# Kernel optimization log

Hardware: AMD Instinct MI355X
Metric: run time of the kernel (lower is better)

The kernel has to match this reference:

```python
import jax, jax.numpy as jnp
import numpy as np

EPS = 1e-6
CHUNK = 128  # chunk size for the chunked causal recurrence


def elu_feature_map(x):
    # fast_transformers default feature map: elu(x) + 1
    return jax.nn.elu(x) + 1.0


def causal_dot_product(Q, K, V):
    """out[l] = Q[l] @ sum_{l' <= l} K[l']^T V[l'].
    Q, K: (N, L, H, E); V: (N, L, H, D) -> (N, L, H, D).
    Chunked parallel recurrence: intra-chunk masked attention + inter-chunk state.
    """
    N, L, H, E = Q.shape
    D = V.shape[-1]
    C = CHUNK
    nc = L // C

    def to_chunks(x):
        # (N, L, H, F) -> (nc, N, H, C, F)
        F = x.shape[-1]
        return x.reshape(N, nc, C, H, F).transpose(1, 0, 3, 2, 4)

    Qc, Kc, Vc = to_chunks(Q), to_chunks(K), to_chunks(V)
    tri = jnp.tril(jnp.ones((C, C), dtype=Q.dtype))  # causal mask within chunk

    def step(state, qkv):  # state: (N, H, E, D)
        q, k, v = qkv  # (N,H,C,E), (N,H,C,E), (N,H,C,D)
        inter = jnp.einsum('nhce,nhed->nhcd', q, state)
        scores = jnp.einsum('nhce,nhfe->nhcf', q, k) * tri
        intra = jnp.einsum('nhcf,nhfd->nhcd', scores, v)
        state = state + jnp.einsum('nhce,nhcd->nhed', k, v)
        return state, inter + intra

    state0 = jnp.zeros((N, H, E, D), dtype=Q.dtype)
    _, out = jax.lax.scan(step, state0, (Qc, Kc, Vc))
    # (nc, N, H, C, D) -> (N, L, H, D)
    return out.transpose(1, 0, 3, 2, 4).reshape(N, L, H, D)


def setup_inputs() -> dict:
    key = jax.random.key(0)
    k1, k2, k3 = jax.random.split(key, 3)
    N, L, H, E = 4, 8192, 16, 64
    return {
        'queries': jax.random.normal(k1, (N, L, H, E), jnp.float32),
        'keys': jax.random.normal(k2, (N, L, H, E), jnp.float32),
        'values': jax.random.normal(k3, (N, L, H, E), jnp.float32),
        'key_mask': jnp.ones((N, L), dtype=bool),
    }


def reference(queries, keys, values, key_mask):
    # key_mask is accepted but unused, matching the original forward().
    Q = elu_feature_map(queries)
    K = elu_feature_map(keys)
    Z = 1.0 / (jnp.einsum('nlhi,nlhi->nlh', Q, jnp.cumsum(K, axis=1)) + EPS)
    V = causal_dot_product(Q, K, values)
    return V * Z[..., None]
```

## Files before the change

### kernel.cpp

```cpp
#include <hip/hip_runtime.h>
#include <hip/hip_bf16.h>


#define Nn   4
#define Ll   8192
#define Hh   16
#define NHh  64
#define CCH  64
#define LDB  72
#define SLOT 4160
#define EPSF 1e-6f

typedef __attribute__((ext_vector_type(8))) short short8;
typedef __attribute__((ext_vector_type(4))) float floatx4;

__device__ __forceinline__ float elu1(float x) {
  return x > 0.f ? x + 1.f : __expf(x);
}

__device__ __forceinline__ float4 elu4(float4 v) {
  v.x = elu1(v.x); v.y = elu1(v.y); v.z = elu1(v.z); v.w = elu1(v.w);
  return v;
}

__device__ __forceinline__ floatx4 mfma16(short8 a, short8 b, floatx4 c) {
  return __builtin_amdgcn_mfma_f32_16x16x32_bf16(a, b, c, 0, 0, 0);
}

__device__ __forceinline__ short8 frag_ld(const __hip_bfloat16* base, int row,
                                          int kh, int quad) {
  return *(const short8*)(base + row * LDB + kh * 32 + quad * 8);
}

__device__ __forceinline__ void st4bf(__hip_bfloat16* dst, float a, float b,
                                      float c, float d) {
  union { __hip_bfloat16 h[4]; uint2 u; } pk;
  pk.h[0] = __float2bfloat16(a); pk.h[1] = __float2bfloat16(b);
  pk.h[2] = __float2bfloat16(c); pk.h[3] = __float2bfloat16(d);
  *(uint2*)dst = pk.u;
}

__device__ __forceinline__ float bf2f(short s) {
  union { unsigned u; float f; } cv;
  cv.u = ((unsigned)(unsigned short)s) << 16;
  return cv.f;
}

__device__ __forceinline__ float sum8bf(short8 v) {
  float s = 0.f;
#pragma unroll
  for (int i = 0; i < 8; ++i) s += bf2f(v[i]);
  return s;
}

__global__ __launch_bounds__(256, 4) void la_pass1(
    const float* __restrict__ Kg, const float* __restrict__ Vg,
    float* __restrict__ ws, int G, int Lseg) {
  const int bid = blockIdx.x;
  const int nh = bid / G, g = bid % G;
  const int n = nh / Hh, h = nh % Hh;
  const int t = threadIdx.x;
  const int wave = t >> 6, lane = t & 63, m = lane & 15, quad = lane >> 4;
  const int jr0 = m * 4;
  const int er0 = wave * 16 + quad * 4;

  __shared__ __hip_bfloat16 Ktb[64 * LDB];
  __shared__ __hip_bfloat16 Vtb[64 * LDB];
  __shared__ float kpart[4][64];

  floatx4 Sacc[4];
  const floatx4 z4 = {0.f, 0.f, 0.f, 0.f};
#pragma unroll
  for (int b = 0; b < 4; ++b) Sacc[b] = z4;
  float ksr = 0.f;

  const int nchunk = Lseg / CCH;
  for (int c = 0; c < nchunk; ++c) {
    const size_t gb =
        ((size_t)((n * Ll + g * Lseg + c * CCH + jr0) * Hh + h)) * 64 + er0;
    float4 k0 = elu4(*(const float4*)(Kg + gb));
    float4 k1 = elu4(*(const float4*)(Kg + gb + 1024));
    float4 k2 = elu4(*(const float4*)(Kg + gb + 2048));
    float4 k3 = elu4(*(const float4*)(Kg + gb + 3072));
    float4 v0 = *(const float4*)(Vg + gb);
    float4 v1 = *(const float4*)(Vg + gb + 1024);
    float4 v2 = *(const float4*)(Vg + gb + 2048);
    float4 v3 = *(const float4*)(Vg + gb + 3072);
    st4bf(&Ktb[(er0 + 0) * LDB + jr0], k0.x, k1.x, k2.x, k3.x);
    st4bf(&Ktb[(er0 + 1) * LDB + jr0], k0.y, k1.y, k2.y, k3.y);
    st4bf(&Ktb[(er0 + 2) * LDB + jr0], k0.z, k1.z, k2.z, k3.z);
    st4bf(&Ktb[(er0 + 3) * LDB + jr0], k0.w, k1.w, k2.w, k3.w);
    st4bf(&Vtb[(er0 + 0) * LDB + jr0], v0.x, v1.x, v2.x, v3.x);
    st4bf(&Vtb[(er0 + 1) * LDB + jr0], v0.y, v1.y, v2.y, v3.y);
    st4bf(&Vtb[(er0 + 2) * LDB + jr0], v0.z, v1.z, v2.z, v3.z);
    st4bf(&Vtb[(er0 + 3) * LDB + jr0], v0.w, v1.w, v2.w, v3.w);
    __syncthreads();

    const short8 a0 = frag_ld(Vtb, 16 * wave + m, 0, quad);
    const short8 a1 = frag_ld(Vtb, 16 * wave + m, 1, quad);
    __builtin_amdgcn_s_setprio(1);
#pragma unroll
    for (int b = 0; b < 4; ++b) {
      Sacc[b] = mfma16(a0, frag_ld(Ktb, 16 * b + m, 0, quad), Sacc[b]);
      Sacc[b] = mfma16(a1, frag_ld(Ktb, 16 * b + m, 1, quad), Sacc[b]);
    }
    __builtin_amdgcn_s_setprio(0);
    {
      const short8 x0 = *(const short8*)(&Ktb[lane * LDB + wave * 16]);
      const short8 x1 = *(const short8*)(&Ktb[lane * LDB + wave * 16 + 8]);
      kpart[wave][lane] = sum8bf(x0) + sum8bf(x1);
    }
    __syncthreads();
    if (t < 64) ksr += kpart[0][t] + kpart[1][t] + kpart[2][t] + kpart[3][t];
  }
  const size_t slot = (size_t)bid * SLOT;
#pragma unroll
  for (int b = 0; b < 4; ++b)
#pragma unroll
    for (int r = 0; r < 4; ++r) {
      const int d = 16 * wave + quad * 4 + r, e = 16 * b + m;
      ws[slot + d * 64 + e] = Sacc[b][r];
    }
  if (t < 64) ws[slot + 4096 + t] = ksr;
}

__global__ __launch_bounds__(256) void la_pass2(float* __restrict__ ws, int G) {
  const int nh = blockIdx.x / 17, part = blockIdx.x % 17;
  const int idx = part * 256 + threadIdx.x;
  if (idx >= SLOT) return;
  float run = 0.f;
  for (int g = 0; g < G; ++g) {
    const size_t base = (size_t)(nh * G + g) * SLOT;
    const float cur = ws[base + idx];
    ws[base + idx] = run;
    run += cur;
  }
}

__global__ __launch_bounds__(256, 4) void la_pass3(
    const float* __restrict__ Qg, const float* __restrict__ Kg,
    const float* __restrict__ Vg, const float* __restrict__ ws,
    float* __restrict__ out, int G, int Lseg, int has_prefix) {
  const int bid = blockIdx.x;
  const int nh = bid / G, g = bid % G;
  const int n = nh / Hh, h = nh % Hh;
  const int t = threadIdx.x;
  const int wave = t >> 6, lane = t & 63, m = lane & 15, quad = lane >> 4;
  const int row = t >> 2, q4 = t & 3;
  const int jr0 = m * 4;
  const int er0 = wave * 16 + quad * 4;

  __shared__ __hip_bfloat16 QPb[64 * LDB];
  __shared__ __hip_bfloat16 Kb [64 * LDB];
  __shared__ __hip_bfloat16 Ktb[64 * LDB];
  __shared__ __hip_bfloat16 Vtb[64 * LDB];
  __shared__ float ksum[64];
  __shared__ float kpart[4][64];

  const size_t slot = (size_t)bid * SLOT;
  floatx4 Sacc[4];
  const floatx4 z4 = {0.f, 0.f, 0.f, 0.f};
#pragma unroll
  for (int b = 0; b < 4; ++b) {
    Sacc[b] = z4;
    if (has_prefix) {
#pragma unroll
      for (int r = 0; r < 4; ++r)
        Sacc[b][r] = ws[slot + (16 * wave + quad * 4 + r) * 64 + 16 * b + m];
    }
  }
  if (t < 64) ksum[t] = has_prefix ? ws[slot + 4096 + t] : 0.f;

  const int nchunk = Lseg / CCH;
  for (int c = 0; c < nchunk; ++c) {
    const int lbase = g * Lseg + c * CCH;
    const size_t gbr = ((size_t)((n * Ll + lbase + row) * Hh + h)) * 64;
#pragma unroll
    for (int u = 0; u < 4; ++u) {
      const int col = u * 16 + q4 * 4;
      float4 qv = elu4(*(const float4*)(Qg + gbr + col));
      float4 kv = elu4(*(const float4*)(Kg + gbr + col));
      st4bf(&QPb[row * LDB + col], qv.x, qv.y, qv.z, qv.w);
      st4bf(&Kb [row * LDB + col], kv.x, kv.y, kv.z, kv.w);
      Ktb[(col + 0) * LDB + row] = __float2bfloat16(kv.x);
      Ktb[(col + 1) * LDB + row] = __float2bfloat16(kv.y);
      Ktb[(col + 2) * LDB + row] = __float2bfloat16(kv.z);
      Ktb[(col + 3) * LDB + row] = __float2bfloat16(kv.w);
    }
    {
      const size_t gbv =
          ((size_t)((n * Ll + lbase + jr0) * Hh + h)) * 64 + er0;
      float4 v0 = *(const float4*)(Vg + gbv);
      float4 v1 = *(const float4*)(Vg + gbv + 1024);
      float4 v2 = *(const float4*)(Vg + gbv + 2048);
      float4 v3 = *(const float4*)(Vg + gbv + 3072);
      st4bf(&Vtb[(er0 + 0) * LDB + jr0], v0.x, v1.x, v2.x, v3.x);
      st4bf(&Vtb[(er0 + 1) * LDB + jr0], v0.y, v1.y, v2.y, v3.y);
      st4bf(&Vtb[(er0 + 2) * LDB + jr0], v0.z, v1.z, v2.z, v3.z);
      st4bf(&Vtb[(er0 + 3) * LDB + jr0], v0.w, v1.w, v2.w, v3.w);
    }
    __syncthreads();

    const short8 qa0 = frag_ld(QPb, 16 * wave + m, 0, quad);
    const short8 qa1 = frag_ld(QPb, 16 * wave + m, 1, quad);
    floatx4 sc[4];
    __builtin_amdgcn_s_setprio(1);
#pragma unroll
    for (int b = 0; b < 4; ++b) {
      sc[b] = mfma16(qa0, frag_ld(Kb, 16 * b + m, 0, quad), z4);
      sc[b] = mfma16(qa1, frag_ld(Kb, 16 * b + m, 1, quad), sc[b]);
    }
    __builtin_amdgcn_s_setprio(0);
    float dpart = 0.f;
    {
      const float* ks0 = &ksum[quad * 8];
      const float* ks1 = &ksum[32 + quad * 8];
#pragma unroll
      for (int u = 0; u < 8; ++u) dpart += bf2f(qa0[u]) * ks0[u];
#pragma unroll
      for (int u = 0; u < 8; ++u) dpart += bf2f(qa1[u]) * ks1[u];
    }
    dpart += __shfl_xor(dpart, 16);
    dpart += __shfl_xor(dpart, 32);
    float z[4];
#pragma unroll
    for (int r = 0; r < 4; ++r) {
      const int i = 16 * wave + quad * 4 + r;
      float rs = 0.f;
#pragma unroll
      for (int b = 0; b < 4; ++b) {
        const int j = 16 * b + m;
        rs += (j <= i) ? sc[b][r] : 0.f;
      }
      rs += __shfl_xor(rs, 1);
      rs += __shfl_xor(rs, 2);
      rs += __shfl_xor(rs, 4);
      rs += __shfl_xor(rs, 8);
      const float den = __shfl(dpart, quad * 4 + r);
      z[r] = 1.f / (den + rs + EPSF);
    }
    __syncthreads();

#pragma unroll
    for (int b = 0; b < 4; ++b)
#pragma unroll
      for (int r = 0; r < 4; ++r) {
        const int i = 16 * wave + quad * 4 + r, j = 16 * b + m;
        QPb[i * LDB + j] = __float2bfloat16(j <= i ? sc[b][r] : 0.f);
        Kb[i * LDB + j] = __float2bfloat16(Sacc[b][r]);
      }
    __syncthreads();

    const short8 pa0 = frag_ld(QPb, 16 * wave + m, 0, quad);
    const short8 pa1 = frag_ld(QPb, 16 * wave + m, 1, quad);
    const short8 va0 = frag_ld(Vtb, 16 * wave + m, 0, quad);
    const short8 va1 = frag_ld(Vtb, 16 * wave + m, 1, quad);
    floatx4 O[4];
    __builtin_amdgcn_s_setprio(1);
#pragma unroll
    for (int b = 0; b < 4; ++b) {
      O[b] = mfma16(qa0, frag_ld(Kb, 16 * b + m, 0, quad), z4);
      O[b] = mfma16(qa1, frag_ld(Kb, 16 * b + m, 1, quad), O[b]);
      O[b] = mfma16(pa0, frag_ld(Vtb, 16 * b + m, 0, quad), O[b]);
      O[b] = mfma16(pa1, frag_ld(Vtb, 16 * b + m, 1, quad), O[b]);
      Sacc[b] = mfma16(va0, frag_ld(Ktb, 16 * b + m, 0, quad), Sacc[b]);
      Sacc[b] = mfma16(va1, frag_ld(Ktb, 16 * b + m, 1, quad), Sacc[b]);
    }
    __builtin_amdgcn_s_setprio(0);
    {
      const short8 x0 = *(const short8*)(&Ktb[lane * LDB + wave * 16]);
      const short8 x1 = *(const short8*)(&Ktb[lane * LDB + wave * 16 + 8]);
      kpart[wave][lane] = sum8bf(x0) + sum8bf(x1);
    }
    const size_t ob = ((size_t)((n * Ll + lbase) * Hh + h)) * 64;
#pragma unroll
    for (int r = 0; r < 4; ++r) {
      const int i = 16 * wave + quad * 4 + r;
#pragma unroll
      for (int b = 0; b < 4; ++b)
        out[ob + (size_t)i * (Hh * 64) + 16 * b + m] = O[b][r] * z[r];
    }
    __syncthreads();
    if (t < 64)
      ksum[t] += kpart[0][t] + kpart[1][t] + kpart[2][t] + kpart[3][t];
  }
}

extern "C" void kernel_launch(void* const* d_in, const int* in_sizes, int n_in,
                              void* d_out, int out_size, void* d_ws, size_t ws_size,
                              hipStream_t stream) {
  (void)in_sizes; (void)n_in; (void)out_size;
  const float* Qg = (const float*)d_in[0];
  const float* Kg = (const float*)d_in[1];
  const float* Vg = (const float*)d_in[2];
  float* out = (float*)d_out;
  float* ws = (float*)d_ws;

  const size_t per_seg = (size_t)NHh * SLOT * sizeof(float);
  int G = 1;
  if (ws_size >= 16 * per_seg) G = 16;
  else if (ws_size >= 8 * per_seg) G = 8;
  else if (ws_size >= 4 * per_seg) G = 4;
  else if (ws_size >= 2 * per_seg) G = 2;
  const int Lseg = Ll / G;

  if (G > 1) {
    la_pass1<<<NHh * G, 256, 0, stream>>>(Kg, Vg, ws, G, Lseg);
    la_pass2<<<NHh * 17, 256, 0, stream>>>(ws, G);
  }
  la_pass3<<<NHh * G, 256, 0, stream>>>(Qg, Kg, Vg, ws, out, G, Lseg, G > 1 ? 1 : 0);
}
```

Before: 480.3 us.

## Double-buffer pass1 chunks with register prefetch and use lgkm-only barriers

Pass1 now prefetches the next chunk's K/V into registers and double-buffers the LDS tiles, so global loads overlap the MFMA work. The K column-sum moves from an LDS reduction into private register sums combined with shuffles at the end. Pass3 issues all Q/K/V global loads up front, defers the V stores to LDS, and both passes replace __syncthreads with a barrier that waits only on LDS counters, letting global loads stay in flight across barriers. The cost is more register pressure and LDS, which could lower occupancy.

```diff
diff --git a/kernel.cpp b/kernel.cpp
--- a/kernel.cpp
+++ b/kernel.cpp
@@ -25,6 +25,12 @@
 
 __device__ __forceinline__ floatx4 mfma16(short8 a, short8 b, floatx4 c) {
   return __builtin_amdgcn_mfma_f32_16x16x32_bf16(a, b, c, 0, 0, 0);
+}
+
+__device__ __forceinline__ void bar_lgkm() {
+  __builtin_amdgcn_s_waitcnt(0xc07f);
+  __builtin_amdgcn_s_barrier();
+  __builtin_amdgcn_sched_barrier(0);
 }
 
 __device__ __forceinline__ short8 frag_ld(const __hip_bfloat16* base, int row,
@@ -64,54 +70,83 @@
   const int jr0 = m * 4;
   const int er0 = wave * 16 + quad * 4;
 
-  __shared__ __hip_bfloat16 Ktb[64 * LDB];
-  __shared__ __hip_bfloat16 Vtb[64 * LDB];
-  __shared__ float kpart[4][64];
+  __shared__ __hip_bfloat16 Kt[2][64 * LDB];
+  __shared__ __hip_bfloat16 Vt[2][64 * LDB];
 
   floatx4 Sacc[4];
   const floatx4 z4 = {0.f, 0.f, 0.f, 0.f};
 #pragma unroll
   for (int b = 0; b < 4; ++b) Sacc[b] = z4;
-  float ksr = 0.f;
+  float kpriv[4] = {0.f, 0.f, 0.f, 0.f};
 
   const int nchunk = Lseg / CCH;
-  for (int c = 0; c < nchunk; ++c) {
-    const size_t gb =
-        ((size_t)((n * Ll + g * Lseg + c * CCH + jr0) * Hh + h)) * 64 + er0;
-    float4 k0 = elu4(*(const float4*)(Kg + gb));
-    float4 k1 = elu4(*(const float4*)(Kg + gb + 1024));
-    float4 k2 = elu4(*(const float4*)(Kg + gb + 2048));
-    float4 k3 = elu4(*(const float4*)(Kg + gb + 3072));
-    float4 v0 = *(const float4*)(Vg + gb);
-    float4 v1 = *(const float4*)(Vg + gb + 1024);
-    float4 v2 = *(const float4*)(Vg + gb + 2048);
-    float4 v3 = *(const float4*)(Vg + gb + 3072);
-    st4bf(&Ktb[(er0 + 0) * LDB + jr0], k0.x, k1.x, k2.x, k3.x);
-    st4bf(&Ktb[(er0 + 1) * LDB + jr0], k0.y, k1.y, k2.y, k3.y);
-    st4bf(&Ktb[(er0 + 2) * LDB + jr0], k0.z, k1.z, k2.z, k3.z);
-    st4bf(&Ktb[(er0 + 3) * LDB + jr0], k0.w, k1.w, k2.w, k3.w);
-    st4bf(&Vtb[(er0 + 0) * LDB + jr0], v0.x, v1.x, v2.x, v3.x);
-    st4bf(&Vtb[(er0 + 1) * LDB + jr0], v0.y, v1.y, v2.y, v3.y);
-    st4bf(&Vtb[(er0 + 2) * LDB + jr0], v0.z, v1.z, v2.z, v3.z);
-    st4bf(&Vtb[(er0 + 3) * LDB + jr0], v0.w, v1.w, v2.w, v3.w);
-    __syncthreads();
-
-    const short8 a0 = frag_ld(Vtb, 16 * wave + m, 0, quad);
-    const short8 a1 = frag_ld(Vtb, 16 * wave + m, 1, quad);
-    __builtin_amdgcn_s_setprio(1);
-#pragma unroll
-    for (int b = 0; b < 4; ++b) {
-      Sacc[b] = mfma16(a0, frag_ld(Ktb, 16 * b + m, 0, quad), Sacc[b]);
-      Sacc[b] = mfma16(a1, frag_ld(Ktb, 16 * b + m, 1, quad), Sacc[b]);
-    }
-    __builtin_amdgcn_s_setprio(0);
-    {
-      const short8 x0 = *(const short8*)(&Ktb[lane * LDB + wave * 16]);
-      const short8 x1 = *(const short8*)(&Ktb[lane * LDB + wave * 16 + 8]);
-      kpart[wave][lane] = sum8bf(x0) + sum8bf(x1);
-    }
-    __syncthreads();
-    if (t < 64) ksr += kpart[0][t] + kpart[1][t] + kpart[2][t] + kpart[3][t];
+
+#define P1_LOAD(KR, VR, c_) do { \
+    const size_t gb_ = \
+        ((size_t)((n * Ll + g * Lseg + (c_) * CCH + jr0) * Hh + h)) * 64 + er0; \
+    KR[0] = *(const float4*)(Kg + gb_);        \
+    KR[1] = *(const float4*)(Kg + gb_ + 1024); \
+    KR[2] = *(const float4*)(Kg + gb_ + 2048); \
+    KR[3] = *(const float4*)(Kg + gb_ + 3072); \
+    VR[0] = *(const float4*)(Vg + gb_);        \
+    VR[1] = *(const float4*)(Vg + gb_ + 1024); \
+    VR[2] = *(const float4*)(Vg + gb_ + 2048); \
+    VR[3] = *(const float4*)(Vg + gb_ + 3072); \
+  } while (0)
+
+#define P1_STAGE(KR, VR, p_) do { \
+    float4 e0 = elu4(KR[0]), e1 = elu4(KR[1]), e2 = elu4(KR[2]), e3 = elu4(KR[3]); \
+    kpriv[0] += e0.x + e1.x + e2.x + e3.x; \
+    kpriv[1] += e0.y + e1.y + e2.y + e3.y; \
+    kpriv[2] += e0.z + e1.z + e2.z + e3.z; \
+    kpriv[3] += e0.w + e1.w + e2.w + e3.w; \
+    __hip_bfloat16* kt_ = Kt[p_]; __hip_bfloat16* vt_ = Vt[p_]; \
+    st4bf(&kt_[(er0 + 0) * LDB + jr0], e0.x, e1.x, e2.x, e3.x); \
+    st4bf(&kt_[(er0 + 1) * LDB + jr0], e0.y, e1.y, e2.y, e3.y); \
+    st4bf(&kt_[(er0 + 2) * LDB + jr0], e0.z, e1.z, e2.z, e3.z); \
+    st4bf(&kt_[(er0 + 3) * LDB + jr0], e0.w, e1.w, e2.w, e3.w); \
+    st4bf(&vt_[(er0 + 0) * LDB + jr0], VR[0].x, VR[1].x, VR[2].x, VR[3].x); \
+    st4bf(&vt_[(er0 + 1) * LDB + jr0], VR[0].y, VR[1].y, VR[2].y, VR[3].y); \
+    st4bf(&vt_[(er0 + 2) * LDB + jr0], VR[0].z, VR[1].z, VR[2].z, VR[3].z); \
+    st4bf(&vt_[(er0 + 3) * LDB + jr0], VR[0].w, VR[1].w, VR[2].w, VR[3].w); \
+  } while (0)
+
+#define P1_MFMA(p_) do { \
+    const short8 a0 = frag_ld(Vt[p_], 16 * wave + m, 0, quad); \
+    const short8 a1 = frag_ld(Vt[p_], 16 * wave + m, 1, quad); \
+    __builtin_amdgcn_s_setprio(1); \
+    _Pragma("unroll") \
+    for (int b = 0; b < 4; ++b) { \
+      Sacc[b] = mfma16(a0, frag_ld(Kt[p_], 16 * b + m, 0, quad), Sacc[b]); \
+      Sacc[b] = mfma16(a1, frag_ld(Kt[p_], 16 * b + m, 1, quad), Sacc[b]); \
+    } \
+    __builtin_amdgcn_s_setprio(0); \
+  } while (0)
+
+  float4 ka[4], va[4], kb[4], vb[4];
+  P1_LOAD(ka, va, 0);
+  P1_LOAD(kb, vb, 1);
+  P1_STAGE(ka, va, 0);
+  for (int c = 0; c < nchunk; c += 2) {
+    if (c + 2 < nchunk) P1_LOAD(ka, va, c + 2);
+    bar_lgkm();
+    P1_MFMA(0);
+    P1_STAGE(kb, vb, 1);
+    if (c + 3 < nchunk) P1_LOAD(kb, vb, c + 3);
+    bar_lgkm();
+    P1_MFMA(1);
+    if (c + 2 < nchunk) P1_STAGE(ka, va, 0);
+  }
+#undef P1_LOAD
+#undef P1_STAGE
+#undef P1_MFMA
+
+#pragma unroll
+  for (int i = 0; i < 4; ++i) {
+    kpriv[i] += __shfl_xor(kpriv[i], 1);
+    kpriv[i] += __shfl_xor(kpriv[i], 2);
+    kpriv[i] += __shfl_xor(kpriv[i], 4);
+    kpriv[i] += __shfl_xor(kpriv[i], 8);
   }
   const size_t slot = (size_t)bid * SLOT;
 #pragma unroll
@@ -121,7 +156,9 @@
       const int d = 16 * wave + quad * 4 + r, e = 16 * b + m;
       ws[slot + d * 64 + e] = Sacc[b][r];
     }
-  if (t < 64) ws[slot + 4096 + t] = ksr;
+  if (m == 0)
+#pragma unroll
+    for (int i = 0; i < 4; ++i) ws[slot + 4096 + er0 + i] = kpriv[i];
 }
 
 __global__ __launch_bounds__(256) void la_pass2(float* __restrict__ ws, int G) {
@@ -175,11 +212,23 @@
   for (int c = 0; c < nchunk; ++c) {
     const int lbase = g * Lseg + c * CCH;
     const size_t gbr = ((size_t)((n * Ll + lbase + row) * Hh + h)) * 64;
+    const size_t gbv = ((size_t)((n * Ll + lbase + jr0) * Hh + h)) * 64 + er0;
+    float4 qr[4], kr[4];
 #pragma unroll
     for (int u = 0; u < 4; ++u) {
       const int col = u * 16 + q4 * 4;
-      float4 qv = elu4(*(const float4*)(Qg + gbr + col));
-      float4 kv = elu4(*(const float4*)(Kg + gbr + col));
+      qr[u] = *(const float4*)(Qg + gbr + col);
+      kr[u] = *(const float4*)(Kg + gbr + col);
+    }
+    float4 vr0 = *(const float4*)(Vg + gbv);
+    float4 vr1 = *(const float4*)(Vg + gbv + 1024);
+    float4 vr2 = *(const float4*)(Vg + gbv + 2048);
+    float4 vr3 = *(const float4*)(Vg + gbv + 3072);
+#pragma unroll
+    for (int u = 0; u < 4; ++u) {
+      const int col = u * 16 + q4 * 4;
+      float4 qv = elu4(qr[u]);
+      float4 kv = elu4(kr[u]);
       st4bf(&QPb[row * LDB + col], qv.x, qv.y, qv.z, qv.w);
       st4bf(&Kb [row * LDB + col], kv.x, kv.y, kv.z, kv.w);
       Ktb[(col + 0) * LDB + row] = __float2bfloat16(kv.x);
@@ -187,19 +236,7 @@
       Ktb[(col + 2) * LDB + row] = __float2bfloat16(kv.z);
       Ktb[(col + 3) * LDB + row] = __float2bfloat16(kv.w);
     }
-    {
-      const size_t gbv =
-          ((size_t)((n * Ll + lbase + jr0) * Hh + h)) * 64 + er0;
-      float4 v0 = *(const float4*)(Vg + gbv);
-      float4 v1 = *(const float4*)(Vg + gbv + 1024);
-      float4 v2 = *(const float4*)(Vg + gbv + 2048);
-      float4 v3 = *(const float4*)(Vg + gbv + 3072);
-      st4bf(&Vtb[(er0 + 0) * LDB + jr0], v0.x, v1.x, v2.x, v3.x);
-      st4bf(&Vtb[(er0 + 1) * LDB + jr0], v0.y, v1.y, v2.y, v3.y);
-      st4bf(&Vtb[(er0 + 2) * LDB + jr0], v0.z, v1.z, v2.z, v3.z);
-      st4bf(&Vtb[(er0 + 3) * LDB + jr0], v0.w, v1.w, v2.w, v3.w);
-    }
-    __syncthreads();
+    bar_lgkm();
 
     const short8 qa0 = frag_ld(QPb, 16 * wave + m, 0, quad);
     const short8 qa1 = frag_ld(QPb, 16 * wave + m, 1, quad);
@@ -239,7 +276,7 @@
       const float den = __shfl(dpart, quad * 4 + r);
       z[r] = 1.f / (den + rs + EPSF);
     }
-    __syncthreads();
+    bar_lgkm();
 
 #pragma unroll
     for (int b = 0; b < 4; ++b)
@@ -249,7 +286,11 @@
         QPb[i * LDB + j] = __float2bfloat16(j <= i ? sc[b][r] : 0.f);
         Kb[i * LDB + j] = __float2bfloat16(Sacc[b][r]);
       }
-    __syncthreads();
+    st4bf(&Vtb[(er0 + 0) * LDB + jr0], vr0.x, vr1.x, vr2.x, vr3.x);
+    st4bf(&Vtb[(er0 + 1) * LDB + jr0], vr0.y, vr1.y, vr2.y, vr3.y);
+    st4bf(&Vtb[(er0 + 2) * LDB + jr0], vr0.z, vr1.z, vr2.z, vr3.z);
+    st4bf(&Vtb[(er0 + 3) * LDB + jr0], vr0.w, vr1.w, vr2.w, vr3.w);
+    bar_lgkm();
 
     const short8 pa0 = frag_ld(QPb, 16 * wave + m, 0, quad);
     const short8 pa1 = frag_ld(QPb, 16 * wave + m, 1, quad);
@@ -280,7 +321,7 @@
       for (int b = 0; b < 4; ++b)
         out[ob + (size_t)i * (Hh * 64) + 16 * b + m] = O[b][r] * z[r];
     }
-    __syncthreads();
+    bar_lgkm();
     if (t < 64)
       ksum[t] += kpart[0][t] + kpart[1][t] + kpart[2][t] + kpart[3][t];
   }
```

After: 481.5 us. About the same (+0.2%).
